# Kernel tuning notes

Measured on AMD Instinct MI355X. Metric: run time of the kernel, lower is better.

## Reference

```python
import jax, jax.numpy as jnp
import numpy as np

B, S, D = 2, 2048, 1024
H, DQK = 16, 64          # n_head, d_qk = d_O // n_head
DV = 64                  # d_v = d_O // n_head
TEMP = DQK ** 0.5
EPS = 1e-6


def relu15(x):
    # ReLU capped at 15 (custom non-softmax attention activation)
    return jnp.clip(x, 0.0, 15.0)


def setup_inputs() -> dict:
    key = jax.random.key(0)
    ks = jax.random.split(key, 10)
    s = 0.02
    return {
        "q": jax.random.normal(ks[0], (B, S, D), jnp.float32),
        "k": jax.random.normal(ks[1], (B, S, D), jnp.float32),
        "v": jax.random.normal(ks[2], (B, S, D), jnp.float32),
        "Wq": jax.random.normal(ks[3], (D, H * DQK), jnp.float32) * s,
        "Wk": jax.random.normal(ks[4], (D, H * DQK), jnp.float32) * s,
        "Wv": jax.random.normal(ks[5], (D, H * DV), jnp.float32) * s,
        "Wfc": jax.random.normal(ks[6], (H * DV, H * DV), jnp.float32) * s,
        "gamma": jnp.ones((H * DV,), jnp.float32),
        "beta": jnp.zeros((H * DV,), jnp.float32),
    }


def reference(q, k, v, Wq, Wk, Wv, Wfc, gamma, beta):
    residual = q                                   # d_Q == d_O path
    # QKV projections (no bias)
    qh = (q @ Wq).reshape(B, S, H, DQK).transpose(0, 2, 1, 3)   # [B,H,S,dqk]
    kh = (k @ Wk).reshape(B, S, H, DQK).transpose(0, 2, 1, 3)
    vh = (v @ Wv).reshape(B, S, H, DV).transpose(0, 2, 1, 3)
    # custom attention: scaled scores -> ReLU15 (no softmax normalization)
    attn = jnp.einsum('bhqd,bhkd->bhqk', qh / TEMP, kh)          # [B,H,S,S]
    attn = relu15(attn)
    o = jnp.einsum('bhqk,bhkd->bhqd', attn, vh)                  # [B,H,S,dv]
    o = o.transpose(0, 2, 1, 3).reshape(B, S, H * DV)            # [B,S,d_O]
    # output projection + residual + LayerNorm
    o = o @ Wfc + residual
    mu = jnp.mean(o, axis=-1, keepdims=True)
    var = jnp.var(o, axis=-1, keepdims=True)
    o = (o - mu) / jnp.sqrt(var + EPS) * gamma + beta
    return o
```

## Files before the change

### kernel.cpp

```cpp
#include <hip/hip_runtime.h>
#include <stdint.h>

#define DEV static __device__ __forceinline__

typedef __attribute__((ext_vector_type(4)))  float f32x4;
typedef __attribute__((ext_vector_type(16))) float f32x16;
typedef __bf16 bf16x8 __attribute__((ext_vector_type(8)));

constexpr int Bc = 2, S = 2048, Dm = 1024, H = 16, DH = 64;
constexpr int BS  = Bc * S;
constexpr int HSZ = Bc * H * S * DH;

constexpr size_t OFF_QKVB  = 0;
constexpr size_t OFF_WT    = 25165824;
constexpr size_t OFF_HEADS = 33554432;
constexpr size_t OFF_VT    = 58720256;
constexpr size_t OFF_O     = 67108864;

DEV uint16_t f2bf(float f) {
    uint32_t u = __float_as_uint(f);
    uint32_t r = u + 0x7FFFu + ((u >> 16) & 1u);
    return (uint16_t)(r >> 16);
}
DEV uint32_t cvtpk(float lo, float hi) {
    uint32_t r;
    asm("v_cvt_pk_bf16_f32 %0, %1, %2" : "=v"(r) : "v"(lo), "v"(hi));
    return r;
}
DEV float clip15(float x, float c15) {
    float r;
    asm("v_med3_f32 %0, %1, 0, %2" : "=v"(r) : "v"(x), "v"(c15));
    return r;
}
DEV uint32_t swz128(uint32_t byteoff) {
    return byteoff ^ (((byteoff >> 7) & 7u) << 4);
}
DEV void gll16(const void* g, void* l) {
    auto gp = (const __attribute__((address_space(1))) uint32_t*)g;
    auto lp = (__attribute__((address_space(3))) uint32_t*)l;
    __builtin_amdgcn_global_load_lds(gp, lp, 16, 0, 0);
}
DEV bf16x8 ld_frag(const char* base, uint32_t logical_off) {
    return __builtin_bit_cast(bf16x8, *(const uint4*)(base + swz128(logical_off)));
}
DEV bf16x8 ld_frag_g(const void* p) {
    return __builtin_bit_cast(bf16x8, *(const uint4*)p);
}

__global__ __launch_bounds__(256) void k_convert(const float* __restrict__ q,
                                                 const float* __restrict__ k,
                                                 const float* __restrict__ v,
                                                 uint16_t* __restrict__ out) {
    const int64_t n1 = (int64_t)BS * Dm;
    int64_t i = ((int64_t)blockIdx.x * 256 + threadIdx.x) * 8;
    const float* src; int64_t j;
    if (i < n1)            { src = q; j = i; }
    else if (i < 2 * n1)   { src = k; j = i - n1; }
    else                   { src = v; j = i - 2 * n1; }
    float4 a = *(const float4*)(src + j);
    float4 b = *(const float4*)(src + j + 4);
    union { uint16_t u[8]; uint4 q4; } o;
    o.u[0] = f2bf(a.x); o.u[1] = f2bf(a.y); o.u[2] = f2bf(a.z); o.u[3] = f2bf(a.w);
    o.u[4] = f2bf(b.x); o.u[5] = f2bf(b.y); o.u[6] = f2bf(b.z); o.u[7] = f2bf(b.w);
    *(uint4*)(out + i) = o.q4;
}

__global__ __launch_bounds__(256) void k_transw(const float* __restrict__ w0,
                                                const float* __restrict__ w1,
                                                const float* __restrict__ w2,
                                                const float* __restrict__ w3,
                                                uint16_t* __restrict__ wt) {
    int mat = blockIdx.y;
    const float* w = (mat == 0) ? w0 : (mat == 1) ? w1 : (mat == 2) ? w2 : w3;
    float scale = (mat == 0) ? 0.125f : 1.0f;
    uint16_t* out = wt + (size_t)mat * 1024 * 1024;
    int tile = blockIdx.x;
    int tr = (tile >> 4) << 6, tc = (tile & 15) << 6;
    __shared__ float lds[64][65];
    int t = threadIdx.x;
#pragma unroll
    for (int p = 0; p < 4; ++p) {
        int r = p * 16 + (t >> 4);
        int c = (t & 15) * 4;
        float4 x = *(const float4*)(w + (size_t)(tr + r) * 1024 + tc + c);
        lds[r][c] = x.x; lds[r][c + 1] = x.y; lds[r][c + 2] = x.z; lds[r][c + 3] = x.w;
    }
    __syncthreads();
    int n = t >> 2, kc = (t & 3) * 16;
    union { uint16_t u[16]; uint4 q[2]; } tt;
#pragma unroll
    for (int j = 0; j < 16; ++j) tt.u[j] = f2bf(lds[kc + j][n] * scale);
    uint16_t* dst = out + (size_t)(tc + n) * 1024 + tr + kc;
    *(uint4*)dst = tt.q[0];
    *(uint4*)(dst + 8) = tt.q[1];
}

struct Acc { f32x4 a[4][4]; };

DEV void stage128(const uint16_t* g, int ldbytes, char* lds) {
    int tid = threadIdx.x;
#pragma unroll
    for (int it = 0; it < 4; ++it) {
        uint32_t p = it * 4096 + tid * 16;
        uint32_t lo = swz128(p);
        uint32_t row = lo >> 7, col = lo & 127;
        gll16((const char*)g + (size_t)row * ldbytes + col,
              lds + it * 4096 + (tid & ~63) * 16);
    }
}

DEV void gemm_core(const uint16_t* Ta, const uint16_t* Tb, int K,
                   char* la, char* lb, Acc& acc) {
    int lane = threadIdx.x & 63, w = threadIdx.x >> 6;
    int wr = w >> 1, wc = w & 1;
#pragma unroll
    for (int ia = 0; ia < 4; ++ia)
#pragma unroll
        for (int ib = 0; ib < 4; ++ib)
#pragma unroll
            for (int r = 0; r < 4; ++r) acc.a[ia][ib][r] = 0.f;
    for (int k0 = 0; k0 < K; k0 += 64) {
        __syncthreads();
        stage128(Ta + k0, K * 2, la);
        stage128(Tb + k0, K * 2, lb);
        __syncthreads();
#pragma unroll
        for (int kk = 0; kk < 2; ++kk) {
            bf16x8 af[4], bfr[4];
#pragma unroll
            for (int ia = 0; ia < 4; ++ia) {
                uint32_t row = wr * 64 + ia * 16 + (lane & 15);
                af[ia] = ld_frag(la, row * 128 + kk * 64 + (lane >> 4) * 16);
            }
#pragma unroll
            for (int ib = 0; ib < 4; ++ib) {
                uint32_t row = wc * 64 + ib * 16 + (lane & 15);
                bfr[ib] = ld_frag(lb, row * 128 + kk * 64 + (lane >> 4) * 16);
            }
#pragma unroll
            for (int ia = 0; ia < 4; ++ia)
#pragma unroll
                for (int ib = 0; ib < 4; ++ib)
                    acc.a[ia][ib] = __builtin_amdgcn_mfma_f32_16x16x32_bf16(
                        af[ia], bfr[ib], acc.a[ia][ib], 0, 0, 0);
        }
    }
}

__global__ __launch_bounds__(256) void k_proj(const uint16_t* __restrict__ qkvb,
                                              const uint16_t* __restrict__ WT,
                                              uint16_t* __restrict__ heads) {
    __shared__ char lds[32768];
    int raw = blockIdx.x;
    int blk = (raw & 7) * 96 + (raw >> 3);
    int sel = blk >> 8;
    int t2 = blk & 255; int bm = t2 >> 3, bn = t2 & 7;
    const uint16_t* Act = qkvb + (size_t)sel * BS * Dm + (size_t)bm * 128 * Dm;
    const uint16_t* Wtt = WT   + (size_t)sel * Dm * Dm + (size_t)bn * 128 * Dm;
    Acc acc;
    gemm_core(Wtt, Act, 1024, lds, lds + 16384, acc);
    uint16_t* out = heads + (size_t)sel * HSZ;
    int lane = threadIdx.x & 63, w = threadIdx.x >> 6;
    int na = bn * 128 + (w >> 1) * 64, mb = bm * 128 + (w & 1) * 64;
#pragma unroll
    for (int ia = 0; ia < 4; ++ia)
#pragma unroll
        for (int ib = 0; ib < 4; ++ib) {
            int n0 = na + ia * 16 + (lane >> 4) * 4;
            int m  = mb + ib * 16 + (lane & 15);
            uint2 d;
            d.x = cvtpk(acc.a[ia][ib][0], acc.a[ia][ib][1]);
            d.y = cvtpk(acc.a[ia][ib][2], acc.a[ia][ib][3]);
            int b = m >> 11, s = m & 2047, h = n0 >> 6, dd = n0 & 63;
            *(uint2*)(out + (((size_t)(b * H + h)) * S + s) * 64 + dd) = d;
        }
}

__global__ __launch_bounds__(256) void k_transv(const uint16_t* __restrict__ Vh,
                                                uint16_t* __restrict__ Vt) {
    int bh = blockIdx.x >> 5, st = blockIdx.x & 31;
    int s0 = st * 64;
    const uint16_t* src = Vh + (size_t)bh * S * 64 + (size_t)s0 * 64;
    uint16_t* dst = Vt + (size_t)bh * 64 * S;
    __shared__ uint16_t lds[64][65];
    int t = threadIdx.x;
    {
        int r = t >> 2, c = (t & 3) * 16;
        union { uint16_t u[16]; uint4 q[2]; } x;
        x.q[0] = *(const uint4*)(src + (size_t)r * 64 + c);
        x.q[1] = *(const uint4*)(src + (size_t)r * 64 + c + 8);
#pragma unroll
        for (int j = 0; j < 16; ++j) lds[r][c + j] = x.u[j];
    }
    __syncthreads();
    {
        int d = t >> 2, sc = (t & 3) * 16;
        union { uint16_t u[16]; uint4 q[2]; } x;
#pragma unroll
        for (int j = 0; j < 16; ++j) x.u[j] = lds[sc + j][d];
        uint16_t* p = dst + (size_t)d * S + s0 + sc;
        *(uint4*)p = x.q[0];
        *(uint4*)(p + 8) = x.q[1];
    }
}

__global__ __launch_bounds__(128) void k_attn(const uint16_t* __restrict__ Qh,
                                              const uint16_t* __restrict__ Kh,
                                              const uint16_t* __restrict__ Vt,
                                              uint16_t* __restrict__ O) {
    __shared__ char kv[3][16384];
    int raw = blockIdx.x;
    int bid = (raw & 7) * 64 + (raw >> 3);
    int bh = bid >> 4, qb = (bid & 15) * 128;
    int tid = threadIdx.x, lane = tid & 63, w = tid >> 6;
    int l31 = lane & 31, hi = lane >> 5;
    const char* Kbase = (const char*)(Kh + (size_t)bh * S * 64);
    const char* Vbase = (const char*)(Vt + (size_t)bh * 64 * S);

    bf16x8 qf[2][4];
#pragma unroll
    for (int qs = 0; qs < 2; ++qs) {
        const char* qrow = (const char*)(Qh + (size_t)bh * S * 64
                                         + (size_t)(qb + w * 64 + qs * 32 + l31) * 64);
#pragma unroll
        for (int ks = 0; ks < 4; ++ks)
            qf[qs][ks] = ld_frag_g(qrow + ks * 32 + hi * 16);
    }
    f32x16 oa[2][2];
#pragma unroll
    for (int qs = 0; qs < 2; ++qs)
#pragma unroll
        for (int nt = 0; nt < 2; ++nt)
#pragma unroll
            for (int r = 0; r < 16; ++r) oa[qs][nt][r] = 0.f;
    float c15 = 15.0f;

    auto stageKV = [&](int tile) {
        int bufi = tile % 3;
        int kv0 = tile * 64;
#pragma unroll
        for (int it = 0; it < 4; ++it) {
            uint32_t p = it * 2048 + tid * 16;
            uint32_t lo = swz128(p);
            uint32_t row = lo >> 7, col = lo & 127;
            gll16(Kbase + (size_t)(kv0 + row) * 128 + col,
                  kv[bufi] + it * 2048 + (tid & ~63) * 16);
            gll16(Vbase + (size_t)row * 4096 + (size_t)kv0 * 2 + col,
                  kv[bufi] + 8192 + it * 2048 + (tid & ~63) * 16);
        }
    };

    stageKV(0);
    stageKV(1);
    for (int t = 0; t < 32; ++t) {
        if (t < 31) { asm volatile("s_waitcnt vmcnt(8)" ::: "memory"); }
        else        { asm volatile("s_waitcnt vmcnt(0)" ::: "memory"); }
        __builtin_amdgcn_sched_barrier(0);
        __builtin_amdgcn_s_barrier();
        const char* kb = kv[t % 3];
        const char* vb = kv[t % 3] + 8192;
        if (t < 30) stageKV(t + 2);
        __builtin_amdgcn_s_setprio(1);
#pragma unroll
        for (int mt = 0; mt < 2; ++mt) {
            bf16x8 kf[4];
#pragma unroll
            for (int ks = 0; ks < 4; ++ks)
                kf[ks] = ld_frag(kb, (mt * 32 + l31) * 128 + ks * 32 + hi * 16);
            bf16x8 pa[2][2];
#pragma unroll
            for (int qs = 0; qs < 2; ++qs) {
                f32x16 c;
#pragma unroll
                for (int r = 0; r < 16; ++r) c[r] = 0.f;
#pragma unroll
                for (int ks = 0; ks < 4; ++ks)
                    c = __builtin_amdgcn_mfma_f32_32x32x16_bf16(kf[ks], qf[qs][ks], c, 0, 0, 0);
#pragma unroll
                for (int r = 0; r < 16; ++r) c[r] = clip15(c[r], c15);
#pragma unroll
                for (int ks2 = 0; ks2 < 2; ++ks2) {
                    union { uint32_t w[4]; bf16x8 v; } up;
#pragma unroll
                    for (int jj = 0; jj < 2; ++jj) {
                        uint32_t sA = cvtpk(c[8 * ks2 + 2 * jj],     c[8 * ks2 + 2 * jj + 1]);
                        uint32_t sB = cvtpk(c[8 * ks2 + 4 + 2 * jj], c[8 * ks2 + 4 + 2 * jj + 1]);
                        asm volatile("v_permlane32_swap_b32 %0, %1" : "+v"(sA), "+v"(sB));
                        up.w[jj] = sA; up.w[2 + jj] = sB;
                    }
                    pa[qs][ks2] = up.v;
                }
            }
#pragma unroll
            for (int ks2 = 0; ks2 < 2; ++ks2)
#pragma unroll
                for (int nt = 0; nt < 2; ++nt) {
                    bf16x8 vbf = ld_frag(vb, (nt * 32 + l31) * 128 + mt * 64 + ks2 * 32 + hi * 16);
#pragma unroll
                    for (int qs = 0; qs < 2; ++qs)
                        oa[qs][nt] = __builtin_amdgcn_mfma_f32_32x32x16_bf16(
                            vbf, pa[qs][ks2], oa[qs][nt], 0, 0, 0);
                }
        }
        __builtin_amdgcn_s_setprio(0);
    }
    int b = bh >> 4, h = bh & 15;
#pragma unroll
    for (int qs = 0; qs < 2; ++qs) {
        int q = qb + w * 64 + qs * 32 + l31;
#pragma unroll
        for (int nt = 0; nt < 2; ++nt)
#pragma unroll
            for (int g = 0; g < 4; ++g) {
                uint2 d;
                d.x = cvtpk(oa[qs][nt][4 * g],     oa[qs][nt][4 * g + 1]);
                d.y = cvtpk(oa[qs][nt][4 * g + 2], oa[qs][nt][4 * g + 3]);
                int col = h * 64 + nt * 32 + 8 * g + 4 * hi;
                *(uint2*)(O + ((size_t)(b * S + q)) * 1024 + col) = d;
            }
    }
}

__global__ __launch_bounds__(256) void k_fc(const uint16_t* __restrict__ Ob,
                                            const uint16_t* __restrict__ WfcT,
                                            const float* __restrict__ resid,
                                            float* __restrict__ out) {
    __shared__ char lds[32768];
    int raw = blockIdx.x;
    int blk = (raw & 7) * 32 + (raw >> 3);
    int bm = blk >> 3, bn = blk & 7;
    const uint16_t* Act = Ob   + (size_t)bm * 128 * Dm;
    const uint16_t* Wtt = WfcT + (size_t)bn * 128 * Dm;
    Acc acc;
    gemm_core(Wtt, Act, 1024, lds, lds + 16384, acc);
    int lane = threadIdx.x & 63, w = threadIdx.x >> 6;
    int na = bn * 128 + (w >> 1) * 64, mb = bm * 128 + (w & 1) * 64;
#pragma unroll
    for (int ia = 0; ia < 4; ++ia)
#pragma unroll
        for (int ib = 0; ib < 4; ++ib) {
            int n0 = na + ia * 16 + (lane >> 4) * 4;
            int m  = mb + ib * 16 + (lane & 15);
            size_t idx = (size_t)m * 1024 + n0;
            float4 r4 = *(const float4*)(resid + idx);
            float4 o;
            o.x = acc.a[ia][ib][0] + r4.x;
            o.y = acc.a[ia][ib][1] + r4.y;
            o.z = acc.a[ia][ib][2] + r4.z;
            o.w = acc.a[ia][ib][3] + r4.w;
            *(float4*)(out + idx) = o;
        }
}

__global__ __launch_bounds__(256) void k_ln(float* __restrict__ io,
                                            const float* __restrict__ gamma,
                                            const float* __restrict__ beta) {
    int row = blockIdx.x;
    float* p = io + (size_t)row * 1024;
    int t = threadIdx.x;
    float4 x = *(const float4*)(p + t * 4);
    float s  = x.x + x.y + x.z + x.w;
    float s2 = x.x * x.x + x.y * x.y + x.z * x.z + x.w * x.w;
#pragma unroll
    for (int o = 32; o > 0; o >>= 1) { s += __shfl_xor(s, o); s2 += __shfl_xor(s2, o); }
    __shared__ float red[8];
    int w = t >> 6, lane = t & 63;
    if (lane == 0) { red[w] = s; red[4 + w] = s2; }
    __syncthreads();
    s  = red[0] + red[1] + red[2] + red[3];
    s2 = red[4] + red[5] + red[6] + red[7];
    float mu  = s * (1.f / 1024.f);
    float var = s2 * (1.f / 1024.f) - mu * mu;
    float inv = rsqrtf(var + 1e-6f);
    float4 g  = *(const float4*)(gamma + t * 4);
    float4 bb = *(const float4*)(beta + t * 4);
    x.x = (x.x - mu) * inv * g.x + bb.x;
    x.y = (x.y - mu) * inv * g.y + bb.y;
    x.z = (x.z - mu) * inv * g.z + bb.z;
    x.w = (x.w - mu) * inv * g.w + bb.w;
    *(float4*)(p + t * 4) = x;
}

extern "C" void kernel_launch(void* const* d_in, const int* in_sizes, int n_in,
                              void* d_out, int out_size, void* d_ws, size_t ws_size,
                              hipStream_t stream) {
    (void)in_sizes; (void)n_in; (void)out_size; (void)ws_size;
    const float* q     = (const float*)d_in[0];
    const float* k     = (const float*)d_in[1];
    const float* v     = (const float*)d_in[2];
    const float* Wq    = (const float*)d_in[3];
    const float* Wk    = (const float*)d_in[4];
    const float* Wv    = (const float*)d_in[5];
    const float* Wfc   = (const float*)d_in[6];
    const float* gamma = (const float*)d_in[7];
    const float* beta  = (const float*)d_in[8];
    char* ws = (char*)d_ws;
    uint16_t* qkvb  = (uint16_t*)(ws + OFF_QKVB);
    uint16_t* WT    = (uint16_t*)(ws + OFF_WT);
    uint16_t* heads = (uint16_t*)(ws + OFF_HEADS);
    uint16_t* Vt    = (uint16_t*)(ws + OFF_VT);
    uint16_t* Ob    = (uint16_t*)(ws + OFF_O);
    float* out = (float*)d_out;

    k_convert<<<dim3(6144), dim3(256), 0, stream>>>(q, k, v, qkvb);
    k_transw <<<dim3(256, 4), dim3(256), 0, stream>>>(Wq, Wk, Wv, Wfc, WT);
    k_proj   <<<dim3(768), dim3(256), 0, stream>>>(qkvb, WT, heads);
    k_transv <<<dim3(1024), dim3(256), 0, stream>>>(heads + 2 * (size_t)HSZ, Vt);
    k_attn   <<<dim3(512), dim3(128), 0, stream>>>(heads, heads + HSZ, Vt, Ob);
    k_fc     <<<dim3(256), dim3(256), 0, stream>>>(Ob, WT + 3 * 1024 * 1024, q, out);
    k_ln     <<<dim3(4096), dim3(256), 0, stream>>>(out, gamma, beta);
}
```

Measured before the change: 252.0 us.

## Split attention KV range across wave pairs and split-K the output projection

The attention kernel now runs 256 threads per block. Two wave pairs each handle half of the KV sequence with their own triple-buffered smaller tiles, and the partial outputs are reduced through LDS before the bf16 store. The FC GEMM is split along K into two halves written as fp32 partials, and the LayerNorm kernel sums the partials with the residual. Both changes double the parallelism for the 512 and 256 block grids on a 256-CU part, at the cost of extra partial-sum traffic and an LDS reduction.

```diff
diff --git a/kernel.cpp b/kernel.cpp
--- a/kernel.cpp
+++ b/kernel.cpp
@@ -109,7 +109,7 @@
     }
 }
 
-DEV void gemm_core(const uint16_t* Ta, const uint16_t* Tb, int K,
+DEV void gemm_core(const uint16_t* Ta, const uint16_t* Tb, int K, int ldbytes,
                    char* la, char* lb, Acc& acc) {
     int lane = threadIdx.x & 63, w = threadIdx.x >> 6;
     int wr = w >> 1, wc = w & 1;
@@ -121,8 +121,8 @@
             for (int r = 0; r < 4; ++r) acc.a[ia][ib][r] = 0.f;
     for (int k0 = 0; k0 < K; k0 += 64) {
         __syncthreads();
-        stage128(Ta + k0, K * 2, la);
-        stage128(Tb + k0, K * 2, lb);
+        stage128(Ta + k0, ldbytes, la);
+        stage128(Tb + k0, ldbytes, lb);
         __syncthreads();
 #pragma unroll
         for (int kk = 0; kk < 2; ++kk) {
@@ -158,7 +158,7 @@
     const uint16_t* Act = qkvb + (size_t)sel * BS * Dm + (size_t)bm * 128 * Dm;
     const uint16_t* Wtt = WT   + (size_t)sel * Dm * Dm + (size_t)bn * 128 * Dm;
     Acc acc;
-    gemm_core(Wtt, Act, 1024, lds, lds + 16384, acc);
+    gemm_core(Wtt, Act, 1024, 2048, lds, lds + 16384, acc);
     uint16_t* out = heads + (size_t)sel * HSZ;
     int lane = threadIdx.x & 63, w = threadIdx.x >> 6;
     int na = bn * 128 + (w >> 1) * 64, mb = bm * 128 + (w & 1) * 64;
@@ -204,15 +204,17 @@
     }
 }
 
-__global__ __launch_bounds__(128) void k_attn(const uint16_t* __restrict__ Qh,
+__global__ __launch_bounds__(256) void k_attn(const uint16_t* __restrict__ Qh,
                                               const uint16_t* __restrict__ Kh,
                                               const uint16_t* __restrict__ Vt,
                                               uint16_t* __restrict__ O) {
-    __shared__ char kv[3][16384];
+    __shared__ char kvbuf[2][3][8192];
     int raw = blockIdx.x;
     int bid = (raw & 7) * 64 + (raw >> 3);
     int bh = bid >> 4, qb = (bid & 15) * 128;
     int tid = threadIdx.x, lane = tid & 63, w = tid >> 6;
+    int wq = w & 1, wsp = w >> 1;
+    int stid = tid & 127;
     int l31 = lane & 31, hi = lane >> 5;
     const char* Kbase = (const char*)(Kh + (size_t)bh * S * 64);
     const char* Vbase = (const char*)(Vt + (size_t)bh * 64 * S);
@@ -221,7 +223,7 @@
 #pragma unroll
     for (int qs = 0; qs < 2; ++qs) {
         const char* qrow = (const char*)(Qh + (size_t)bh * S * 64
-                                         + (size_t)(qb + w * 64 + qs * 32 + l31) * 64);
+                                         + (size_t)(qb + wq * 64 + qs * 32 + l31) * 64);
 #pragma unroll
         for (int ks = 0; ks < 4; ++ks)
             qf[qs][ks] = ld_frag_g(qrow + ks * 32 + hi * 16);
@@ -235,104 +237,130 @@
             for (int r = 0; r < 16; ++r) oa[qs][nt][r] = 0.f;
     float c15 = 15.0f;
 
-    auto stageKV = [&](int tile) {
-        int bufi = tile % 3;
-        int kv0 = tile * 64;
-#pragma unroll
-        for (int it = 0; it < 4; ++it) {
-            uint32_t p = it * 2048 + tid * 16;
+    auto stageKV = [&](int tl) {
+        int kv0 = wsp * 1024 + tl * 32;
+        char* base = (char*)kvbuf + wsp * 24576 + (tl % 3) * 8192;
+#pragma unroll
+        for (int it = 0; it < 2; ++it) {
+            uint32_t p = it * 2048 + stid * 16;
             uint32_t lo = swz128(p);
             uint32_t row = lo >> 7, col = lo & 127;
             gll16(Kbase + (size_t)(kv0 + row) * 128 + col,
-                  kv[bufi] + it * 2048 + (tid & ~63) * 16);
-            gll16(Vbase + (size_t)row * 4096 + (size_t)kv0 * 2 + col,
-                  kv[bufi] + 8192 + it * 2048 + (tid & ~63) * 16);
+                  base + it * 2048 + (stid & ~63) * 16);
+        }
+#pragma unroll
+        for (int it = 0; it < 2; ++it) {
+            uint32_t p = it * 2048 + stid * 16;
+            uint32_t lo = swz128(p);
+            uint32_t row = lo >> 7, col = lo & 127;
+            uint32_t dv = row + (col >> 6) * 32, kvb = col & 63;
+            gll16(Vbase + (size_t)dv * 4096 + (size_t)kv0 * 2 + kvb,
+                  base + 4096 + it * 2048 + (stid & ~63) * 16);
         }
     };
 
     stageKV(0);
     stageKV(1);
     for (int t = 0; t < 32; ++t) {
-        if (t < 31) { asm volatile("s_waitcnt vmcnt(8)" ::: "memory"); }
+        if (t < 31) { asm volatile("s_waitcnt vmcnt(4)" ::: "memory"); }
         else        { asm volatile("s_waitcnt vmcnt(0)" ::: "memory"); }
         __builtin_amdgcn_sched_barrier(0);
         __builtin_amdgcn_s_barrier();
-        const char* kb = kv[t % 3];
-        const char* vb = kv[t % 3] + 8192;
+        const char* kb = (const char*)kvbuf + wsp * 24576 + (t % 3) * 8192;
+        const char* vb = kb + 4096;
         if (t < 30) stageKV(t + 2);
         __builtin_amdgcn_s_setprio(1);
-#pragma unroll
-        for (int mt = 0; mt < 2; ++mt) {
-            bf16x8 kf[4];
+        bf16x8 kf[4];
+#pragma unroll
+        for (int ks = 0; ks < 4; ++ks)
+            kf[ks] = ld_frag(kb, l31 * 128 + ks * 32 + hi * 16);
+        bf16x8 pa[2][2];
+#pragma unroll
+        for (int qs = 0; qs < 2; ++qs) {
+            f32x16 c;
+#pragma unroll
+            for (int r = 0; r < 16; ++r) c[r] = 0.f;
 #pragma unroll
             for (int ks = 0; ks < 4; ++ks)
-                kf[ks] = ld_frag(kb, (mt * 32 + l31) * 128 + ks * 32 + hi * 16);
-            bf16x8 pa[2][2];
-#pragma unroll
-            for (int qs = 0; qs < 2; ++qs) {
-                f32x16 c;
-#pragma unroll
-                for (int r = 0; r < 16; ++r) c[r] = 0.f;
-#pragma unroll
-                for (int ks = 0; ks < 4; ++ks)
-                    c = __builtin_amdgcn_mfma_f32_32x32x16_bf16(kf[ks], qf[qs][ks], c, 0, 0, 0);
-#pragma unroll
-                for (int r = 0; r < 16; ++r) c[r] = clip15(c[r], c15);
-#pragma unroll
-                for (int ks2 = 0; ks2 < 2; ++ks2) {
-                    union { uint32_t w[4]; bf16x8 v; } up;
-#pragma unroll
-                    for (int jj = 0; jj < 2; ++jj) {
-                        uint32_t sA = cvtpk(c[8 * ks2 + 2 * jj],     c[8 * ks2 + 2 * jj + 1]);
-                        uint32_t sB = cvtpk(c[8 * ks2 + 4 + 2 * jj], c[8 * ks2 + 4 + 2 * jj + 1]);
-                        asm volatile("v_permlane32_swap_b32 %0, %1" : "+v"(sA), "+v"(sB));
-                        up.w[jj] = sA; up.w[2 + jj] = sB;
-                    }
-                    pa[qs][ks2] = up.v;
+                c = __builtin_amdgcn_mfma_f32_32x32x16_bf16(kf[ks], qf[qs][ks], c, 0, 0, 0);
+#pragma unroll
+            for (int r = 0; r < 16; ++r) c[r] = clip15(c[r], c15);
+#pragma unroll
+            for (int ks2 = 0; ks2 < 2; ++ks2) {
+                union { uint32_t w[4]; bf16x8 v; } up;
+#pragma unroll
+                for (int jj = 0; jj < 2; ++jj) {
+                    uint32_t sA = cvtpk(c[8 * ks2 + 2 * jj],     c[8 * ks2 + 2 * jj + 1]);
+                    uint32_t sB = cvtpk(c[8 * ks2 + 4 + 2 * jj], c[8 * ks2 + 4 + 2 * jj + 1]);
+                    asm volatile("v_permlane32_swap_b32 %0, %1" : "+v"(sA), "+v"(sB));
+                    up.w[jj] = sA; up.w[2 + jj] = sB;
                 }
-            }
-#pragma unroll
-            for (int ks2 = 0; ks2 < 2; ++ks2)
-#pragma unroll
-                for (int nt = 0; nt < 2; ++nt) {
-                    bf16x8 vbf = ld_frag(vb, (nt * 32 + l31) * 128 + mt * 64 + ks2 * 32 + hi * 16);
-#pragma unroll
-                    for (int qs = 0; qs < 2; ++qs)
-                        oa[qs][nt] = __builtin_amdgcn_mfma_f32_32x32x16_bf16(
-                            vbf, pa[qs][ks2], oa[qs][nt], 0, 0, 0);
+                pa[qs][ks2] = up.v;
+            }
+        }
+#pragma unroll
+        for (int ks2 = 0; ks2 < 2; ++ks2)
+#pragma unroll
+            for (int nt = 0; nt < 2; ++nt) {
+                bf16x8 vf = ld_frag(vb, l31 * 128 + nt * 64 + ks2 * 32 + hi * 16);
+#pragma unroll
+                for (int qs = 0; qs < 2; ++qs)
+                    oa[qs][nt] = __builtin_amdgcn_mfma_f32_32x32x16_bf16(
+                        vf, pa[qs][ks2], oa[qs][nt], 0, 0, 0);
+            }
+        __builtin_amdgcn_s_setprio(0);
+    }
+    __syncthreads();
+    float* xch = (float*)kvbuf;
+    float* xp = xch + (size_t)(wq * 64 + lane) * 68;
+    if (wsp == 1) {
+#pragma unroll
+        for (int qs = 0; qs < 2; ++qs)
+#pragma unroll
+            for (int nt = 0; nt < 2; ++nt) {
+                union { f32x16 v; float4 q4[4]; } u; u.v = oa[qs][nt];
+#pragma unroll
+                for (int r4 = 0; r4 < 4; ++r4)
+                    *(float4*)(xp + qs * 32 + nt * 16 + r4 * 4) = u.q4[r4];
+            }
+    }
+    __syncthreads();
+    if (wsp == 0) {
+        int b = bh >> 4, h = bh & 15;
+#pragma unroll
+        for (int qs = 0; qs < 2; ++qs) {
+            int q = qb + wq * 64 + qs * 32 + l31;
+#pragma unroll
+            for (int nt = 0; nt < 2; ++nt) {
+#pragma unroll
+                for (int r = 0; r < 16; ++r)
+                    oa[qs][nt][r] += xp[qs * 32 + nt * 16 + r];
+#pragma unroll
+                for (int g = 0; g < 4; ++g) {
+                    uint2 d;
+                    d.x = cvtpk(oa[qs][nt][4 * g],     oa[qs][nt][4 * g + 1]);
+                    d.y = cvtpk(oa[qs][nt][4 * g + 2], oa[qs][nt][4 * g + 3]);
+                    int col = h * 64 + nt * 32 + 8 * g + 4 * hi;
+                    *(uint2*)(O + ((size_t)(b * S + q)) * 1024 + col) = d;
                 }
-        }
-        __builtin_amdgcn_s_setprio(0);
-    }
-    int b = bh >> 4, h = bh & 15;
-#pragma unroll
-    for (int qs = 0; qs < 2; ++qs) {
-        int q = qb + w * 64 + qs * 32 + l31;
-#pragma unroll
-        for (int nt = 0; nt < 2; ++nt)
-#pragma unroll
-            for (int g = 0; g < 4; ++g) {
-                uint2 d;
-                d.x = cvtpk(oa[qs][nt][4 * g],     oa[qs][nt][4 * g + 1]);
-                d.y = cvtpk(oa[qs][nt][4 * g + 2], oa[qs][nt][4 * g + 3]);
-                int col = h * 64 + nt * 32 + 8 * g + 4 * hi;
-                *(uint2*)(O + ((size_t)(b * S + q)) * 1024 + col) = d;
-            }
+            }
+        }
     }
 }
 
 __global__ __launch_bounds__(256) void k_fc(const uint16_t* __restrict__ Ob,
                                             const uint16_t* __restrict__ WfcT,
-                                            const float* __restrict__ resid,
-                                            float* __restrict__ out) {
+                                            float* __restrict__ part) {
     __shared__ char lds[32768];
     int raw = blockIdx.x;
-    int blk = (raw & 7) * 32 + (raw >> 3);
-    int bm = blk >> 3, bn = blk & 7;
-    const uint16_t* Act = Ob   + (size_t)bm * 128 * Dm;
-    const uint16_t* Wtt = WfcT + (size_t)bn * 128 * Dm;
+    int blk = (raw & 7) * 64 + (raw >> 3);
+    int ks = blk >> 8;
+    int t2 = blk & 255; int bm = t2 >> 3, bn = t2 & 7;
+    const uint16_t* Act = Ob   + (size_t)bm * 128 * Dm + ks * 512;
+    const uint16_t* Wtt = WfcT + (size_t)bn * 128 * Dm + ks * 512;
     Acc acc;
-    gemm_core(Wtt, Act, 1024, lds, lds + 16384, acc);
+    gemm_core(Wtt, Act, 512, 2048, lds, lds + 16384, acc);
+    float* o = part + (size_t)ks * BS * Dm;
     int lane = threadIdx.x & 63, w = threadIdx.x >> 6;
     int na = bn * 128 + (w >> 1) * 64, mb = bm * 128 + (w & 1) * 64;
 #pragma unroll
@@ -342,23 +370,28 @@
             int n0 = na + ia * 16 + (lane >> 4) * 4;
             int m  = mb + ib * 16 + (lane & 15);
             size_t idx = (size_t)m * 1024 + n0;
-            float4 r4 = *(const float4*)(resid + idx);
-            float4 o;
-            o.x = acc.a[ia][ib][0] + r4.x;
-            o.y = acc.a[ia][ib][1] + r4.y;
-            o.z = acc.a[ia][ib][2] + r4.z;
-            o.w = acc.a[ia][ib][3] + r4.w;
-            *(float4*)(out + idx) = o;
-        }
-}
-
-__global__ __launch_bounds__(256) void k_ln(float* __restrict__ io,
+            float4 v;
+            v.x = acc.a[ia][ib][0]; v.y = acc.a[ia][ib][1];
+            v.z = acc.a[ia][ib][2]; v.w = acc.a[ia][ib][3];
+            *(float4*)(o + idx) = v;
+        }
+}
+
+__global__ __launch_bounds__(256) void k_ln(const float* __restrict__ p0,
+                                            const float* __restrict__ p1,
+                                            const float* __restrict__ resid,
                                             const float* __restrict__ gamma,
-                                            const float* __restrict__ beta) {
+                                            const float* __restrict__ beta,
+                                            float* __restrict__ out) {
     int row = blockIdx.x;
-    float* p = io + (size_t)row * 1024;
+    size_t off = (size_t)row * 1024 + threadIdx.x * 4;
     int t = threadIdx.x;
-    float4 x = *(const float4*)(p + t * 4);
+    float4 a = *(const float4*)(p0 + off);
+    float4 b2 = *(const float4*)(p1 + off);
+    float4 r = *(const float4*)(resid + off);
+    float4 x;
+    x.x = a.x + b2.x + r.x; x.y = a.y + b2.y + r.y;
+    x.z = a.z + b2.z + r.z; x.w = a.w + b2.w + r.w;
     float s  = x.x + x.y + x.z + x.w;
     float s2 = x.x * x.x + x.y * x.y + x.z * x.z + x.w * x.w;
 #pragma unroll
@@ -378,7 +411,7 @@
     x.y = (x.y - mu) * inv * g.y + bb.y;
     x.z = (x.z - mu) * inv * g.z + bb.z;
     x.w = (x.w - mu) * inv * g.w + bb.w;
-    *(float4*)(p + t * 4) = x;
+    *(float4*)(out + off) = x;
 }
 
 extern "C" void kernel_launch(void* const* d_in, const int* in_sizes, int n_in,
@@ -400,13 +433,15 @@
     uint16_t* heads = (uint16_t*)(ws + OFF_HEADS);
     uint16_t* Vt    = (uint16_t*)(ws + OFF_VT);
     uint16_t* Ob    = (uint16_t*)(ws + OFF_O);
+    float* fcpart   = (float*)(ws + OFF_HEADS);
     float* out = (float*)d_out;
 
     k_convert<<<dim3(6144), dim3(256), 0, stream>>>(q, k, v, qkvb);
     k_transw <<<dim3(256, 4), dim3(256), 0, stream>>>(Wq, Wk, Wv, Wfc, WT);
     k_proj   <<<dim3(768), dim3(256), 0, stream>>>(qkvb, WT, heads);
     k_transv <<<dim3(1024), dim3(256), 0, stream>>>(heads + 2 * (size_t)HSZ, Vt);
-    k_attn   <<<dim3(512), dim3(128), 0, stream>>>(heads, heads + HSZ, Vt, Ob);
-    k_fc     <<<dim3(256), dim3(256), 0, stream>>>(Ob, WT + 3 * 1024 * 1024, q, out);
-    k_ln     <<<dim3(4096), dim3(256), 0, stream>>>(out, gamma, beta);
-}
+    k_attn   <<<dim3(512), dim3(256), 0, stream>>>(heads, heads + HSZ, Vt, Ob);
+    k_fc     <<<dim3(512), dim3(256), 0, stream>>>(Ob, WT + 3 * 1024 * 1024, fcpart);
+    k_ln     <<<dim3(4096), dim3(256), 0, stream>>>(fcpart, fcpart + (size_t)BS * Dm,
+                                                    q, gamma, beta, out);
+}
```

Result: faster. 232.9 us (-7.6%).
